# Optimization experiments

Measured on AMD Instinct MI355X. Metric: run time of the kernel, lower is better.

Reference implementation:

```python
import jax, jax.numpy as jnp
import numpy as np

N, C, H, W = 16, 512, 32, 32
NH = 8            # num_heads
HD = C // NH      # head dim c = 64
G = C // 4        # GroupNorm groups = 128
EPS = 1e-5


def conv1x1(X, Wt, b):
    # 1x1 Conv2d == per-pixel linear over channels
    return jnp.einsum('oc,nchw->nohw', Wt, X) + b[None, :, None, None]


def setup_inputs() -> dict:
    key = jax.random.key(0)
    ks = jax.random.split(key, 9)
    s = 0.02
    inp = {
        'X': jax.random.normal(ks[0], (N, C, H, W), jnp.float32),
        'Wq': jax.random.normal(ks[1], (C, C), jnp.float32) * s,
        'bq': jax.random.normal(ks[2], (C,), jnp.float32) * s,
        'Wk': jax.random.normal(ks[3], (C, C), jnp.float32) * s,
        'bk': jax.random.normal(ks[4], (C,), jnp.float32) * s,
        'Wv': jax.random.normal(ks[5], (C, C), jnp.float32) * s,
        'bv': jax.random.normal(ks[6], (C,), jnp.float32) * s,
        'Wo': jax.random.normal(ks[7], (C, C), jnp.float32) * s,
        'bo': jax.random.normal(ks[8], (C,), jnp.float32) * s,
        'gn_w': jnp.ones((C,), jnp.float32),
        'gn_b': jnp.zeros((C,), jnp.float32),
    }
    return inp


def reference(X, Wq, bq, Wk, bk, Wv, bv, Wo, bo, gn_w, gn_b):
    # NOTE: original torch code does  K, Q, V = (Q_conv(X), K_conv(X), V_conv(X))
    # i.e. K gets the Q_conv weights and Q gets the K_conv weights; mirror that.
    K = conv1x1(X, Wq, bq)
    Q = conv1x1(X, Wk, bk)
    V = conv1x1(X, Wv, bv)

    d = H * W
    Kh = K.reshape(N, NH, HD, d)  # [n,h,c,d]
    Qh = Q.reshape(N, NH, HD, d)
    Vh = V.reshape(N, NH, HD, d)

    # softmax-free channel attention: (Q^T K) then V (Q^T K)^T
    A = jnp.einsum('nhcd,nhcD->nhdD', Qh, Kh)   # [n,h,d,d]
    O = jnp.einsum('nhdD,nhcD->nhcd', A, Vh)    # [n,h,c,d]

    O = O.reshape(N, C, H, W)
    O = conv1x1(O, Wo, bo)

    # GroupNorm(G, C) with affine, eps=1e-5
    Og = O.reshape(N, G, C // G, H, W)
    mu = Og.mean(axis=(2, 3, 4), keepdims=True)
    var = Og.var(axis=(2, 3, 4), keepdims=True)
    On = ((Og - mu) * jax.lax.rsqrt(var + EPS)).reshape(N, C, H, W)
    On = On * gn_w[None, :, None, None] + gn_b[None, :, None, None]

    return On + X
```

## Files before the change

### kernel.cpp

```cpp
#include <hip/hip_runtime.h>
#include <hip/hip_bf16.h>

typedef __attribute__((ext_vector_type(8))) short s8v;
typedef __attribute__((ext_vector_type(4))) float f32x4;

#define MFMA_BF16 __builtin_amdgcn_mfma_f32_16x16x32_bf16

__device__ inline void gload_lds16(const __hip_bfloat16* g, __hip_bfloat16* l) {
  __builtin_amdgcn_global_load_lds(
      (const __attribute__((address_space(1))) void*)g,
      (__attribute__((address_space(3))) void*)l, 16, 0, 0);
}

__device__ inline void storeC(float* p, float v) { *p = v; }
__device__ inline void storeC(__hip_bfloat16* p, float v) { *p = __float2bfloat16(v); }

__global__ __launch_bounds__(256) void xt_conv(const float* __restrict__ X,
                                               __hip_bfloat16* __restrict__ XT) {
  __shared__ float tl[32][33];
  const int n = blockIdx.z;
  const int c0 = blockIdx.y * 32, p0 = blockIdx.x * 32;
  const int tx = threadIdx.x, ty = threadIdx.y;
  const float* Xp = X + ((long)n * 512 + c0) * 1024 + p0;
#pragma unroll
  for (int i = 0; i < 4; ++i) tl[ty + i * 8][tx] = Xp[(ty + i * 8) * 1024 + tx];
  __syncthreads();
  __hip_bfloat16* XTp = XT + ((long)n * 1024 + p0) * 512 + c0;
#pragma unroll
  for (int i = 0; i < 4; ++i)
    XTp[(ty + i * 8) * 512 + tx] = __float2bfloat16(tl[tx][ty + i * 8]);
}

__global__ __launch_bounds__(256) void wconv(const float* __restrict__ Wq,
                                             const float* __restrict__ Wv,
                                             const float* __restrict__ Wk,
                                             const float* __restrict__ Wo,
                                             const float* __restrict__ bq,
                                             const float* __restrict__ bv,
                                             __hip_bfloat16* __restrict__ WA,
                                             __hip_bfloat16* __restrict__ Wkb,
                                             __hip_bfloat16* __restrict__ WOb,
                                             float* __restrict__ biasKV) {
  const int i = blockIdx.x * 256 + threadIdx.x;
  WA[i] = __float2bfloat16(Wq[i]);
  WA[262144 + i] = __float2bfloat16(Wv[i]);
  Wkb[i] = __float2bfloat16(Wk[i]);
  WOb[i] = __float2bfloat16(Wo[i]);
  if (i < 512) { biasKV[i] = bq[i]; biasKV[512 + i] = bv[i]; }
}

template <typename OutT, bool BROW, bool BCOL>
__global__ __launch_bounds__(256) void gemm_nt(
    const __hip_bfloat16* __restrict__ A, long strideA,
    const __hip_bfloat16* __restrict__ B, long strideB,
    OutT* __restrict__ C, long strideC, int K, int ldc,
    const float* __restrict__ brow, const float* __restrict__ bcol) {
  A += blockIdx.z * strideA;
  B += blockIdx.z * strideB;
  C += blockIdx.z * strideC;
  const int m0 = blockIdx.y * 128;
  const int n0 = blockIdx.x * 128;
  const int tid = threadIdx.x;
  const int wid = tid >> 6, lane = tid & 63;
  const int wm = wid >> 1, wn = wid & 1;

  __shared__ __hip_bfloat16 As[128 * 64];
  __shared__ __hip_bfloat16 Bs[128 * 64];

  f32x4 acc[4][4] = {};

  const __hip_bfloat16* gA0 = A + (long)(m0 + wid * 32 + (lane >> 3)) * K + (lane & 7) * 8;
  const __hip_bfloat16* gB0 = B + (long)(n0 + wid * 32 + (lane >> 3)) * K + (lane & 7) * 8;

  for (int k0 = 0; k0 < K; k0 += 64) {
#pragma unroll
    for (int t = 0; t < 4; ++t) {
      gload_lds16(gA0 + (long)t * 8 * K + k0, &As[(wid * 32 + t * 8) * 64]);
      gload_lds16(gB0 + (long)t * 8 * K + k0, &Bs[(wid * 32 + t * 8) * 64]);
    }
    __syncthreads();
#pragma unroll
    for (int ks = 0; ks < 2; ++ks) {
      const int koff = ks * 32 + (lane >> 4) * 8;
      s8v a[4], b[4];
#pragma unroll
      for (int i = 0; i < 4; ++i)
        a[i] = *(const s8v*)&As[(wm * 64 + i * 16 + (lane & 15)) * 64 + koff];
#pragma unroll
      for (int j = 0; j < 4; ++j)
        b[j] = *(const s8v*)&Bs[(wn * 64 + j * 16 + (lane & 15)) * 64 + koff];
#pragma unroll
      for (int i = 0; i < 4; ++i)
#pragma unroll
        for (int j = 0; j < 4; ++j)
          acc[i][j] = MFMA_BF16(a[i], b[j], acc[i][j], 0, 0, 0);
    }
    __syncthreads();
  }

  const int cr = (lane >> 4) * 4;
  const int cc = lane & 15;
#pragma unroll
  for (int i = 0; i < 4; ++i) {
#pragma unroll
    for (int r = 0; r < 4; ++r) {
      const int gm = m0 + wm * 64 + i * 16 + cr + r;
      const float rb = BROW ? brow[gm] : 0.f;
#pragma unroll
      for (int j = 0; j < 4; ++j) {
        const int gn = n0 + wn * 64 + j * 16 + cc;
        const float cb = BCOL ? bcol[gn] : 0.f;
        storeC(&C[(long)gm * ldc + gn], acc[i][j][r] + rb + cb);
      }
    }
  }
}

__global__ __launch_bounds__(256) void gemm_vkT(const __hip_bfloat16* __restrict__ V,
                                                const __hip_bfloat16* __restrict__ Kk,
                                                __hip_bfloat16* __restrict__ Mt) {
  const int n = blockIdx.x >> 3, h = blockIdx.x & 7;
  const int tid = threadIdx.x, wid = tid >> 6, lane = tid & 63;
  f32x4 acc[4][4] = {};
  const long colbase = (long)n * 1024 + wid * 256 + (lane >> 4) * 8;
  const __hip_bfloat16* Vb = V + (long)(h * 64 + (lane & 15)) * 16384 + colbase;
  const __hip_bfloat16* Kb = Kk + (long)(h * 64 + (lane & 15)) * 16384 + colbase;
  for (int kk = 0; kk < 256; kk += 32) {
    s8v a[4], b[4];
#pragma unroll
    for (int i = 0; i < 4; ++i) a[i] = *(const s8v*)(Vb + (long)i * 16 * 16384 + kk);
#pragma unroll
    for (int j = 0; j < 4; ++j) b[j] = *(const s8v*)(Kb + (long)j * 16 * 16384 + kk);
#pragma unroll
    for (int i = 0; i < 4; ++i)
#pragma unroll
      for (int j = 0; j < 4; ++j) acc[i][j] = MFMA_BF16(a[i], b[j], acc[i][j], 0, 0, 0);
  }
  __shared__ float part[4][4096];
  const int cr = (lane >> 4) * 4, cc = lane & 15;
#pragma unroll
  for (int i = 0; i < 4; ++i)
#pragma unroll
    for (int r = 0; r < 4; ++r)
#pragma unroll
      for (int j = 0; j < 4; ++j)
        part[wid][(i * 16 + cr + r) * 64 + j * 16 + cc] = acc[i][j][r];
  __syncthreads();
  __hip_bfloat16* out = Mt + ((long)n * 8 + h) * 4096;
  for (int e = tid; e < 4096; e += 256) {
    const float sum = part[0][e] + part[1][e] + part[2][e] + part[3][e];
    out[(e & 63) * 64 + (e >> 6)] = __float2bfloat16(sum);
  }
}

__global__ __launch_bounds__(256) void wprime_mfma(const __hip_bfloat16* __restrict__ WOb,
                                                   const __hip_bfloat16* __restrict__ Mt,
                                                   __hip_bfloat16* __restrict__ Wp) {
  const int rt = blockIdx.x, h = blockIdx.y, n = blockIdx.z;
  const int tid = threadIdx.x, wid = tid >> 6, lane = tid & 63;
  const int row0 = rt * 256 + wid * 64;
  f32x4 acc[4][4] = {};
  const __hip_bfloat16* Ab =
      WOb + (long)(row0 + (lane & 15)) * 512 + h * 64 + (lane >> 4) * 8;
  const __hip_bfloat16* Bb =
      Mt + (((long)(n * 8 + h)) * 64 + (lane & 15)) * 64 + (lane >> 4) * 8;
#pragma unroll
  for (int ks = 0; ks < 2; ++ks) {
    s8v a[4], b[4];
#pragma unroll
    for (int i = 0; i < 4; ++i) a[i] = *(const s8v*)(Ab + (long)i * 16 * 512 + ks * 32);
#pragma unroll
    for (int j = 0; j < 4; ++j) b[j] = *(const s8v*)(Bb + (long)j * 16 * 64 + ks * 32);
#pragma unroll
    for (int i = 0; i < 4; ++i)
#pragma unroll
      for (int j = 0; j < 4; ++j) acc[i][j] = MFMA_BF16(a[i], b[j], acc[i][j], 0, 0, 0);
  }
  const int cr = (lane >> 4) * 4, cc = lane & 15;
#pragma unroll
  for (int i = 0; i < 4; ++i)
#pragma unroll
    for (int r = 0; r < 4; ++r)
#pragma unroll
      for (int j = 0; j < 4; ++j)
        Wp[((long)n * 512 + (row0 + i * 16 + cr + r)) * 512 + h * 64 + j * 16 + cc] =
            __float2bfloat16(acc[i][j][r]);
}

__global__ __launch_bounds__(256) void gn_res(const __hip_bfloat16* __restrict__ Y,
                                              const float* __restrict__ X,
                                              const float* __restrict__ gw,
                                              const float* __restrict__ gb,
                                              float* __restrict__ out) {
  const int n = blockIdx.x >> 7, g = blockIdx.x & 127;
  const long base = ((long)n * 512 + g * 4) * 1024;
  const int tid = threadIdx.x;
  float v[16];
  float s = 0.f, s2 = 0.f;
#pragma unroll
  for (int i = 0; i < 2; ++i) {
    const s8v x = *(const s8v*)&Y[base + ((long)(i * 256 + tid)) * 8];
#pragma unroll
    for (int e = 0; e < 8; ++e) {
      const float f = __bfloat162float(((const __hip_bfloat16*)&x)[e]);
      v[i * 8 + e] = f;
      s += f;
      s2 += f * f;
    }
  }
#pragma unroll
  for (int off = 32; off; off >>= 1) {
    s += __shfl_down(s, off);
    s2 += __shfl_down(s2, off);
  }
  __shared__ float rs[8];
  const int wid = tid >> 6, lane = tid & 63;
  if (lane == 0) { rs[wid] = s; rs[4 + wid] = s2; }
  __syncthreads();
  if (tid == 0) {
    const float ts = rs[0] + rs[1] + rs[2] + rs[3];
    const float t2 = rs[4] + rs[5] + rs[6] + rs[7];
    const float mu = ts * (1.f / 4096.f);
    const float var = t2 * (1.f / 4096.f) - mu * mu;
    rs[0] = mu;
    rs[1] = rsqrtf(var + 1e-5f);
  }
  __syncthreads();
  const float mu = rs[0], rstd = rs[1];
#pragma unroll
  for (int i = 0; i < 2; ++i) {
    const int chunk = i * 256 + tid;
    const long e0 = base + (long)chunk * 8;
#pragma unroll
    for (int e = 0; e < 8; ++e) {
      const int c = g * 4 + ((chunk * 8 + e) >> 10);
      out[e0 + e] = (v[i * 8 + e] - mu) * rstd * gw[c] + gb[c] + X[e0 + e];
    }
  }
}

extern "C" void kernel_launch(void* const* d_in, const int* in_sizes, int n_in,
                              void* d_out, int out_size, void* d_ws, size_t ws_size,
                              hipStream_t stream) {
  const float* X  = (const float*)d_in[0];
  const float* Wq = (const float*)d_in[1];
  const float* bq = (const float*)d_in[2];
  const float* Wk = (const float*)d_in[3];
  const float* bk = (const float*)d_in[4];
  const float* Wv = (const float*)d_in[5];
  const float* bv = (const float*)d_in[6];
  const float* Wo = (const float*)d_in[7];
  const float* bo = (const float*)d_in[8];
  const float* gw = (const float*)d_in[9];
  const float* gb = (const float*)d_in[10];
  float* out = (float*)d_out;

  char* ws = (char*)d_ws;
  __hip_bfloat16* XT  = (__hip_bfloat16*)(ws + 0);
  __hip_bfloat16* KV  = (__hip_bfloat16*)(ws + 16777216);
  __hip_bfloat16* QT  = (__hip_bfloat16*)(ws + 50331648);
  __hip_bfloat16* WP  = (__hip_bfloat16*)(ws + 67108864);
  __hip_bfloat16* Mt  = (__hip_bfloat16*)(ws + 75497472);
  __hip_bfloat16* WA  = (__hip_bfloat16*)(ws + 76546048);
  __hip_bfloat16* WKb = (__hip_bfloat16*)(ws + 77594624);
  __hip_bfloat16* WOb = (__hip_bfloat16*)(ws + 78118912);
  float*          bKV = (float*)(ws + 78643200);
  __hip_bfloat16* Y   = (__hip_bfloat16*)(ws + 0);

  xt_conv<<<dim3(32, 16, 16), dim3(32, 8), 0, stream>>>(X, XT);
  wconv<<<1024, 256, 0, stream>>>(Wq, Wv, Wk, Wo, bq, bv, WA, WKb, WOb, bKV);
  gemm_nt<__hip_bfloat16, true, false><<<dim3(128, 8, 1), 256, 0, stream>>>(
      WA, 0, XT, 0, KV, 0, 512, 16384, bKV, nullptr);
  gemm_nt<__hip_bfloat16, false, true><<<dim3(4, 128, 1), 256, 0, stream>>>(
      XT, 0, WKb, 0, QT, 0, 512, 512, nullptr, bk);
  gemm_vkT<<<128, 256, 0, stream>>>(KV + (long)512 * 16384, KV, Mt);
  wprime_mfma<<<dim3(2, 8, 16), 256, 0, stream>>>(WOb, Mt, WP);
  gemm_nt<__hip_bfloat16, true, false><<<dim3(8, 4, 16), 256, 0, stream>>>(
      WP, 262144, QT, 524288, Y, 524288, 512, 1024, bo, nullptr);
  gn_res<<<2048, 256, 0, stream>>>(Y, X, gw, gb, out);
}
```

Measured before the change: 118.5 us.

## Fold Wk into per-batch output weights and vectorize transpose and GN kernels

```diff
diff --git a/kernel.cpp b/kernel.cpp
--- a/kernel.cpp
+++ b/kernel.cpp
@@ -2,6 +2,7 @@
 #include <hip/hip_bf16.h>
 
 typedef __attribute__((ext_vector_type(8))) short s8v;
+typedef __attribute__((ext_vector_type(4))) short s4v;
 typedef __attribute__((ext_vector_type(4))) float f32x4;
 
 #define MFMA_BF16 __builtin_amdgcn_mfma_f32_16x16x32_bf16
@@ -12,23 +13,39 @@
       (__attribute__((address_space(3))) void*)l, 16, 0, 0);
 }
 
+__device__ inline short f2bs(float x) {
+  __hip_bfloat16 b = __float2bfloat16(x);
+  return *reinterpret_cast<short*>(&b);
+}
+
 __device__ inline void storeC(float* p, float v) { *p = v; }
 __device__ inline void storeC(__hip_bfloat16* p, float v) { *p = __float2bfloat16(v); }
 
 __global__ __launch_bounds__(256) void xt_conv(const float* __restrict__ X,
                                                __hip_bfloat16* __restrict__ XT) {
-  __shared__ float tl[32][33];
+  __shared__ float tl[64][65];
   const int n = blockIdx.z;
-  const int c0 = blockIdx.y * 32, p0 = blockIdx.x * 32;
-  const int tx = threadIdx.x, ty = threadIdx.y;
+  const int c0 = blockIdx.y * 64, p0 = blockIdx.x * 64;
+  const int tid = threadIdx.x;
+  const int lr = tid >> 4, lc4 = (tid & 15) * 4;
   const float* Xp = X + ((long)n * 512 + c0) * 1024 + p0;
 #pragma unroll
-  for (int i = 0; i < 4; ++i) tl[ty + i * 8][tx] = Xp[(ty + i * 8) * 1024 + tx];
+  for (int i = 0; i < 4; ++i) {
+    const int ch = i * 16 + lr;
+    const float4 v = *(const float4*)&Xp[(long)ch * 1024 + lc4];
+    tl[ch][lc4 + 0] = v.x; tl[ch][lc4 + 1] = v.y;
+    tl[ch][lc4 + 2] = v.z; tl[ch][lc4 + 3] = v.w;
+  }
   __syncthreads();
   __hip_bfloat16* XTp = XT + ((long)n * 1024 + p0) * 512 + c0;
 #pragma unroll
-  for (int i = 0; i < 4; ++i)
-    XTp[(ty + i * 8) * 512 + tx] = __float2bfloat16(tl[tx][ty + i * 8]);
+  for (int i = 0; i < 4; ++i) {
+    const int px = i * 16 + lr;
+    s4v o;
+#pragma unroll
+    for (int e = 0; e < 4; ++e) o[e] = f2bs(tl[lc4 + e][px]);
+    *(s4v*)&XTp[(long)px * 512 + lc4] = o;
+  }
 }
 
 __global__ __launch_bounds__(256) void wconv(const float* __restrict__ Wq,
@@ -38,23 +55,23 @@
                                              const float* __restrict__ bq,
                                              const float* __restrict__ bv,
                                              __hip_bfloat16* __restrict__ WA,
-                                             __hip_bfloat16* __restrict__ Wkb,
+                                             __hip_bfloat16* __restrict__ WkT,
                                              __hip_bfloat16* __restrict__ WOb,
                                              float* __restrict__ biasKV) {
   const int i = blockIdx.x * 256 + threadIdx.x;
   WA[i] = __float2bfloat16(Wq[i]);
   WA[262144 + i] = __float2bfloat16(Wv[i]);
-  Wkb[i] = __float2bfloat16(Wk[i]);
   WOb[i] = __float2bfloat16(Wo[i]);
+  WkT[i] = __float2bfloat16(Wk[(i & 511) * 512 + (i >> 9)]);
   if (i < 512) { biasKV[i] = bq[i]; biasKV[512 + i] = bv[i]; }
 }
 
-template <typename OutT, bool BROW, bool BCOL>
+template <typename OutT, bool BROW>
 __global__ __launch_bounds__(256) void gemm_nt(
     const __hip_bfloat16* __restrict__ A, long strideA,
     const __hip_bfloat16* __restrict__ B, long strideB,
     OutT* __restrict__ C, long strideC, int K, int ldc,
-    const float* __restrict__ brow, const float* __restrict__ bcol) {
+    const float* __restrict__ brow, long strideBrow) {
   A += blockIdx.z * strideA;
   B += blockIdx.z * strideB;
   C += blockIdx.z * strideC;
@@ -105,27 +122,27 @@
 #pragma unroll
     for (int r = 0; r < 4; ++r) {
       const int gm = m0 + wm * 64 + i * 16 + cr + r;
-      const float rb = BROW ? brow[gm] : 0.f;
+      const float rb = BROW ? brow[blockIdx.z * strideBrow + gm] : 0.f;
 #pragma unroll
       for (int j = 0; j < 4; ++j) {
         const int gn = n0 + wn * 64 + j * 16 + cc;
-        const float cb = BCOL ? bcol[gn] : 0.f;
-        storeC(&C[(long)gm * ldc + gn], acc[i][j][r] + rb + cb);
+        storeC(&C[(long)gm * ldc + gn], acc[i][j][r] + rb);
       }
     }
   }
 }
 
-__global__ __launch_bounds__(256) void gemm_vkT(const __hip_bfloat16* __restrict__ V,
+__global__ __launch_bounds__(512) void gemm_vkT(const __hip_bfloat16* __restrict__ V,
                                                 const __hip_bfloat16* __restrict__ Kk,
                                                 __hip_bfloat16* __restrict__ Mt) {
   const int n = blockIdx.x >> 3, h = blockIdx.x & 7;
   const int tid = threadIdx.x, wid = tid >> 6, lane = tid & 63;
   f32x4 acc[4][4] = {};
-  const long colbase = (long)n * 1024 + wid * 256 + (lane >> 4) * 8;
+  const long colbase = (long)n * 1024 + wid * 128 + (lane >> 4) * 8;
   const __hip_bfloat16* Vb = V + (long)(h * 64 + (lane & 15)) * 16384 + colbase;
   const __hip_bfloat16* Kb = Kk + (long)(h * 64 + (lane & 15)) * 16384 + colbase;
-  for (int kk = 0; kk < 256; kk += 32) {
+#pragma unroll
+  for (int kk = 0; kk < 128; kk += 32) {
     s8v a[4], b[4];
 #pragma unroll
     for (int i = 0; i < 4; ++i) a[i] = *(const s8v*)(Vb + (long)i * 16 * 16384 + kk);
@@ -138,18 +155,30 @@
   }
   __shared__ float part[4][4096];
   const int cr = (lane >> 4) * 4, cc = lane & 15;
-#pragma unroll
-  for (int i = 0; i < 4; ++i)
-#pragma unroll
-    for (int r = 0; r < 4; ++r)
-#pragma unroll
-      for (int j = 0; j < 4; ++j)
-        part[wid][(i * 16 + cr + r) * 64 + j * 16 + cc] = acc[i][j][r];
-  __syncthreads();
-  __hip_bfloat16* out = Mt + ((long)n * 8 + h) * 4096;
-  for (int e = tid; e < 4096; e += 256) {
+  if (wid < 4) {
+#pragma unroll
+    for (int i = 0; i < 4; ++i)
+#pragma unroll
+      for (int r = 0; r < 4; ++r)
+#pragma unroll
+        for (int j = 0; j < 4; ++j)
+          part[wid][(i * 16 + cr + r) * 64 + j * 16 + cc] = acc[i][j][r];
+  }
+  __syncthreads();
+  if (wid >= 4) {
+#pragma unroll
+    for (int i = 0; i < 4; ++i)
+#pragma unroll
+      for (int r = 0; r < 4; ++r)
+#pragma unroll
+        for (int j = 0; j < 4; ++j)
+          part[wid - 4][(i * 16 + cr + r) * 64 + j * 16 + cc] += acc[i][j][r];
+  }
+  __syncthreads();
+  __hip_bfloat16* outp = Mt + ((long)n * 8 + h) * 4096;
+  for (int e = tid; e < 4096; e += 512) {
     const float sum = part[0][e] + part[1][e] + part[2][e] + part[3][e];
-    out[(e & 63) * 64 + (e >> 6)] = __float2bfloat16(sum);
+    outp[(e & 63) * 64 + (e >> 6)] = __float2bfloat16(sum);
   }
 }
 
@@ -187,6 +216,25 @@
             __float2bfloat16(acc[i][j][r]);
 }
 
+__global__ __launch_bounds__(256) void bias2k(const __hip_bfloat16* __restrict__ Wp,
+                                              const float* __restrict__ bk,
+                                              const float* __restrict__ bo,
+                                              float* __restrict__ b2) {
+  const int r = blockIdx.x * 4 + (threadIdx.x >> 6);
+  const int lane = threadIdx.x & 63;
+  const s8v w = *(const s8v*)&Wp[(long)r * 512 + lane * 8];
+  const float4 k0 = *(const float4*)&bk[lane * 8];
+  const float4 k1 = *(const float4*)&bk[lane * 8 + 4];
+  const __hip_bfloat16* wb = (const __hip_bfloat16*)&w;
+  float s = __bfloat162float(wb[0]) * k0.x + __bfloat162float(wb[1]) * k0.y +
+            __bfloat162float(wb[2]) * k0.z + __bfloat162float(wb[3]) * k0.w +
+            __bfloat162float(wb[4]) * k1.x + __bfloat162float(wb[5]) * k1.y +
+            __bfloat162float(wb[6]) * k1.z + __bfloat162float(wb[7]) * k1.w;
+#pragma unroll
+  for (int off = 32; off; off >>= 1) s += __shfl_down(s, off);
+  if (lane == 0) b2[r] = s + bo[r & 511];
+}
+
 __global__ __launch_bounds__(256) void gn_res(const __hip_bfloat16* __restrict__ Y,
                                               const float* __restrict__ X,
                                               const float* __restrict__ gw,
@@ -231,11 +279,21 @@
   for (int i = 0; i < 2; ++i) {
     const int chunk = i * 256 + tid;
     const long e0 = base + (long)chunk * 8;
-#pragma unroll
-    for (int e = 0; e < 8; ++e) {
-      const int c = g * 4 + ((chunk * 8 + e) >> 10);
-      out[e0 + e] = (v[i * 8 + e] - mu) * rstd * gw[c] + gb[c] + X[e0 + e];
-    }
+    const int c = g * 4 + (chunk >> 7);
+    const float sc = rstd * gw[c], sh = gb[c];
+    const float4 x0 = *(const float4*)&X[e0];
+    const float4 x1 = *(const float4*)&X[e0 + 4];
+    float4 o0, o1;
+    o0.x = (v[i * 8 + 0] - mu) * sc + sh + x0.x;
+    o0.y = (v[i * 8 + 1] - mu) * sc + sh + x0.y;
+    o0.z = (v[i * 8 + 2] - mu) * sc + sh + x0.z;
+    o0.w = (v[i * 8 + 3] - mu) * sc + sh + x0.w;
+    o1.x = (v[i * 8 + 4] - mu) * sc + sh + x1.x;
+    o1.y = (v[i * 8 + 5] - mu) * sc + sh + x1.y;
+    o1.z = (v[i * 8 + 6] - mu) * sc + sh + x1.z;
+    o1.w = (v[i * 8 + 7] - mu) * sc + sh + x1.w;
+    *(float4*)&out[e0] = o0;
+    *(float4*)&out[e0 + 4] = o1;
   }
 }
 
@@ -258,24 +316,26 @@
   char* ws = (char*)d_ws;
   __hip_bfloat16* XT  = (__hip_bfloat16*)(ws + 0);
   __hip_bfloat16* KV  = (__hip_bfloat16*)(ws + 16777216);
-  __hip_bfloat16* QT  = (__hip_bfloat16*)(ws + 50331648);
-  __hip_bfloat16* WP  = (__hip_bfloat16*)(ws + 67108864);
-  __hip_bfloat16* Mt  = (__hip_bfloat16*)(ws + 75497472);
-  __hip_bfloat16* WA  = (__hip_bfloat16*)(ws + 76546048);
-  __hip_bfloat16* WKb = (__hip_bfloat16*)(ws + 77594624);
-  __hip_bfloat16* WOb = (__hip_bfloat16*)(ws + 78118912);
-  float*          bKV = (float*)(ws + 78643200);
-  __hip_bfloat16* Y   = (__hip_bfloat16*)(ws + 0);
-
-  xt_conv<<<dim3(32, 16, 16), dim3(32, 8), 0, stream>>>(X, XT);
-  wconv<<<1024, 256, 0, stream>>>(Wq, Wv, Wk, Wo, bq, bv, WA, WKb, WOb, bKV);
-  gemm_nt<__hip_bfloat16, true, false><<<dim3(128, 8, 1), 256, 0, stream>>>(
-      WA, 0, XT, 0, KV, 0, 512, 16384, bKV, nullptr);
-  gemm_nt<__hip_bfloat16, false, true><<<dim3(4, 128, 1), 256, 0, stream>>>(
-      XT, 0, WKb, 0, QT, 0, 512, 512, nullptr, bk);
-  gemm_vkT<<<128, 256, 0, stream>>>(KV + (long)512 * 16384, KV, Mt);
+  __hip_bfloat16* Y   = (__hip_bfloat16*)(ws + 16777216);
+  __hip_bfloat16* WP  = (__hip_bfloat16*)(ws + 50331648);
+  __hip_bfloat16* WPP = (__hip_bfloat16*)(ws + 58720256);
+  __hip_bfloat16* Mt  = (__hip_bfloat16*)(ws + 67108864);
+  __hip_bfloat16* WA  = (__hip_bfloat16*)(ws + 68157440);
+  __hip_bfloat16* WkT = (__hip_bfloat16*)(ws + 69206016);
+  __hip_bfloat16* WOb = (__hip_bfloat16*)(ws + 69730304);
+  float*          bKV = (float*)(ws + 70254592);
+  float*          b2  = (float*)(ws + 70258688);
+
+  xt_conv<<<dim3(16, 8, 16), 256, 0, stream>>>(X, XT);
+  wconv<<<1024, 256, 0, stream>>>(Wq, Wv, Wk, Wo, bq, bv, WA, WkT, WOb, bKV);
+  gemm_nt<__hip_bfloat16, true><<<dim3(128, 8, 1), 256, 0, stream>>>(
+      WA, 0, XT, 0, KV, 0, 512, 16384, bKV, 0);
+  gemm_vkT<<<128, 512, 0, stream>>>(KV + (long)512 * 16384, KV, Mt);
   wprime_mfma<<<dim3(2, 8, 16), 256, 0, stream>>>(WOb, Mt, WP);
-  gemm_nt<__hip_bfloat16, true, false><<<dim3(8, 4, 16), 256, 0, stream>>>(
-      WP, 262144, QT, 524288, Y, 524288, 512, 1024, bo, nullptr);
+  bias2k<<<2048, 256, 0, stream>>>(WP, bk, bo, b2);
+  gemm_nt<__hip_bfloat16, false><<<dim3(4, 4, 16), 256, 0, stream>>>(
+      WP, 262144, WkT, 0, WPP, 262144, 512, 512, nullptr, 0);
+  gemm_nt<__hip_bfloat16, true><<<dim3(8, 4, 16), 256, 0, stream>>>(
+      WPP, 262144, XT, 524288, Y, 524288, 512, 1024, b2, 512);
   gn_res<<<2048, 256, 0, stream>>>(Y, X, gw, gb, out);
 }
```

Measured after the change: 117.5 us. Within noise of the previous version (-0.9%).
